# Kernel tuning notes

Measured on AMD Instinct MI355X. Metric: run time of the kernel, lower is better.

The kernel has to match this reference:

```python
import jax, jax.numpy as jnp
import numpy as np

N, D_IN, D_KQ, D_V = 4096, 1024, 1024, 1024


def setup_inputs() -> dict:
    key = jax.random.key(0)
    kx, kq, kk, kv = jax.random.split(key, 4)
    return {
        "x": jax.random.normal(kx, (N, D_IN), dtype=jnp.float32),
        "W_query": jax.random.uniform(kq, (D_IN, D_KQ), dtype=jnp.float32),
        "W_key": jax.random.uniform(kk, (D_IN, D_KQ), dtype=jnp.float32),
        "W_value": jax.random.uniform(kv, (D_IN, D_V), dtype=jnp.float32),
        "masked": 1,
    }


def reference(x, W_query, W_key, W_value, masked):
    # x: [N, d_in]; single-head, unbatched attention
    queries = x @ W_query          # [N, d_kq]
    keys = x @ W_key               # [N, d_kq]
    values = x @ W_value           # [N, d_v]
    scores = queries @ keys.T      # [N, N]
    if masked:  # masked is a static Python int
        n = x.shape[0]
        causal = jnp.triu(jnp.ones((n, n), dtype=bool), k=1)
        scores = jnp.where(causal, -jnp.inf, scores)
    scale = 1.0 / jnp.sqrt(jnp.asarray(W_key.shape[1], dtype=scores.dtype))
    attn = jax.nn.softmax(scores * scale, axis=-1)
    return attn @ values           # [N, d_v]
```

## Files before the change

kernel.cpp:

```cpp
#include <hip/hip_runtime.h>
#include <hip/hip_bf16.h>


using bf16 = __hip_bfloat16;
using f32x4 = __attribute__((ext_vector_type(4))) float;
using i32x4 = __attribute__((ext_vector_type(4))) int;
using i8 = signed char;

__device__ __forceinline__ void gload_lds16(const void* g, void* l) {
  __builtin_amdgcn_global_load_lds(
      (const __attribute__((address_space(1))) void*)g,
      (__attribute__((address_space(3))) void*)l, 16, 0, 0);
}

template <int ROWS, int CPR, int NT>
__device__ __forceinline__ void stage_tile8(const i8* __restrict__ g, i8* s,
                                            int ld) {
  const int t = threadIdx.x;
#pragma unroll
  for (int c = 0; c < ROWS * CPR / NT; ++c) {
    const int idx = c * NT + t;
    const int row = idx / CPR;
    const int ch = idx & (CPR - 1);
    const int cg = ch ^ ((row >> 1) & (CPR - 1));
    gload_lds16(g + (size_t)row * ld + cg * 16, s + idx * 16);
  }
}
template <int CPR>
__device__ __forceinline__ i32x4 frag_at8(const i8* s, int row, int ch) {
  return *(const i32x4*)&s[(row * CPR + (ch ^ ((row >> 1) & (CPR - 1)))) * 16];
}

__device__ __forceinline__ i32x4 mfma_i8(i32x4 a, i32x4 b, i32x4 c) {
  return __builtin_amdgcn_mfma_i32_16x16x64_i8(a, b, c, 0, 0, 0);
}

__device__ __forceinline__ void wait_vm6() {
  asm volatile("s_waitcnt vmcnt(6)" ::: "memory");
}
__device__ __forceinline__ void wait_vm3() {
  asm volatile("s_waitcnt vmcnt(3)" ::: "memory");
}
__device__ __forceinline__ void wait_vm0() {
  asm volatile("s_waitcnt vmcnt(0)" ::: "memory");
}
__device__ __forceinline__ void barrier_pipe() {
  __builtin_amdgcn_s_barrier();
  __builtin_amdgcn_sched_barrier(0);
}

__global__ __launch_bounds__(256, 3) void gemm_qkv_i8(
    const i8* __restrict__ xh, const i8* __restrict__ xl,
    const i8* __restrict__ qTh, const i8* __restrict__ qTl,
    const i8* __restrict__ kTh, const i8* __restrict__ kTl,
    const i8* __restrict__ vTh, const i8* __restrict__ vTl,
    const float* __restrict__ srow, i8* __restrict__ Qh, i8* __restrict__ Ql,
    i8* __restrict__ Kh, i8* __restrict__ Kl, i8* __restrict__ VT) {
  __shared__ __align__(16) i8 sAh[2][128 * 64], sAl[2][128 * 64];
  __shared__ __align__(16) i8 sBh[2][64 * 64], sBl[2][64 * 64];

  const int bx = blockIdx.x;
  const int which = bx >> 4;
  const int n0 = (bx & 15) * 64;
  const int m0 = blockIdx.y * 128;
  const i8* Bh = which == 0 ? qTh : which == 1 ? kTh : vTh;
  const i8* Bl = which == 0 ? qTl : which == 1 ? kTl : vTl;
  const i8* A_h = xh + (size_t)m0 * 1024;
  const i8* A_l = xl + (size_t)m0 * 1024;
  const i8* B_h = Bh + (size_t)n0 * 1024;
  const i8* B_l = Bl + (size_t)n0 * 1024;

  const int t = threadIdx.x, lane = t & 63, w = t >> 6;
  const int wr = (w >> 1) * 64, wc = (w & 1) * 32;
  const int frow = lane & 15, fc = lane >> 4;

  i32x4 a0[4][2], a1[4][2];
#pragma unroll
  for (int i = 0; i < 4; ++i)
#pragma unroll
    for (int j = 0; j < 2; ++j) {
      a0[i][j] = (i32x4){0, 0, 0, 0};
      a1[i][j] = (i32x4){0, 0, 0, 0};
    }

  auto stage_all = [&](int kt, int b) {
    const int k0 = kt * 64;
    stage_tile8<128, 4, 256>(A_h + k0, sAh[b], 1024);
    stage_tile8<64, 4, 256>(B_h + k0, sBh[b], 1024);
    stage_tile8<128, 4, 256>(A_l + k0, sAl[b], 1024);
    stage_tile8<64, 4, 256>(B_l + k0, sBl[b], 1024);
  };

  stage_all(0, 0);
  for (int kt = 0; kt < 16; ++kt) {
    const int cur = kt & 1;
    if (kt < 15) {
      stage_all(kt + 1, cur ^ 1);
      wait_vm6();
    } else {
      wait_vm0();
    }
    barrier_pipe();

    i32x4 ah[4], al[4], bh[2], bl[2];
#pragma unroll
    for (int i = 0; i < 4; ++i) {
      ah[i] = frag_at8<4>(sAh[cur], wr + i * 16 + frow, fc);
      al[i] = frag_at8<4>(sAl[cur], wr + i * 16 + frow, fc);
    }
#pragma unroll
    for (int j = 0; j < 2; ++j) {
      bh[j] = frag_at8<4>(sBh[cur], wc + j * 16 + frow, fc);
      bl[j] = frag_at8<4>(sBl[cur], wc + j * 16 + frow, fc);
    }

    __builtin_amdgcn_s_setprio(1);
#pragma unroll
    for (int i = 0; i < 4; ++i)
#pragma unroll
      for (int j = 0; j < 2; ++j) {
        a0[i][j] = mfma_i8(ah[i], bh[j], a0[i][j]);
        a1[i][j] = mfma_i8(ah[i], bl[j], a1[i][j]);
        a1[i][j] = mfma_i8(al[i], bh[j], a1[i][j]);
      }
    __builtin_amdgcn_s_setprio(0);
    barrier_pipe();
  }

  const int er = (lane >> 4) * 4, ec = lane & 15;
  if (which < 2) {
    i8* Ph = which == 0 ? Qh : Kh;
    i8* Pl = which == 0 ? Ql : Kl;
#pragma unroll
    for (int i = 0; i < 4; ++i)
#pragma unroll
      for (int j = 0; j < 2; ++j)
#pragma unroll
        for (int r = 0; r < 4; ++r) {
          const int gm = m0 + wr + i * 16 + er + r;
          const int gn = n0 + wc + j * 16 + ec;
          const float Qf =
              65536.f * (float)a0[i][j][r] + 256.f * (float)a1[i][j][r];
          int q16 = __float2int_rn(Qf * (1.f / 262144.f));
          q16 = min(max(q16, -32511), 32511);
          const int h = (q16 + 128) >> 8;
          const int l = q16 - (h << 8);
          const size_t off = (size_t)gm * 1024 + gn;
          Ph[off] = (i8)h;
          Pl[off] = (i8)l;
        }
  } else {
    const int gm_base = m0 + wr;
#pragma unroll
    for (int i = 0; i < 4; ++i)
#pragma unroll
      for (int j = 0; j < 2; ++j) {
        const int gn = n0 + wc + j * 16 + ec;
        uint pk = 0;
#pragma unroll
        for (int r = 0; r < 4; ++r) {
          const int gm = gm_base + i * 16 + er + r;
          const float Vf =
              (65536.f * (float)a0[i][j][r] + 256.f * (float)a1[i][j][r]) *
                  (1.f / 134217728.f) +
              0.5f * srow[gm];
          int v8 = __float2int_rn(Vf);
          v8 = min(max(v8, -127), 127);
          pk |= (uint)(v8 & 255) << (8 * r);
        }
        *(uint*)(VT + (size_t)gn * 4096 + gm_base + i * 16 + er) = pk;
      }
  }
}

__global__ __launch_bounds__(256, 3) void gemm_s_i8(
    const i8* __restrict__ Qh, const i8* __restrict__ Ql,
    const i8* __restrict__ Kh, const i8* __restrict__ Kl,
    const float* __restrict__ srow, const float* __restrict__ qsum,
    const float* __restrict__ ksum, float* __restrict__ S) {
  const int u = blockIdx.x;
  int rb = (int)((sqrtf(4.f * (float)u + 1.f) - 1.f) * 0.5f);
  while ((rb + 1) * (rb + 2) <= u) ++rb;
  while (rb * (rb + 1) > u) --rb;
  const int cb = u - rb * (rb + 1);
  const int n0 = cb * 64, m0 = rb * 128;
  __shared__ __align__(16) i8 sAh[2][128 * 64], sAl[2][128 * 64];
  __shared__ __align__(16) i8 sBh[2][64 * 64], sBl[2][64 * 64];

  const i8* A_h = Qh + (size_t)m0 * 1024;
  const i8* A_l = Ql + (size_t)m0 * 1024;
  const i8* B_h = Kh + (size_t)n0 * 1024;
  const i8* B_l = Kl + (size_t)n0 * 1024;

  const int t = threadIdx.x, lane = t & 63, w = t >> 6;
  const int wr = (w >> 1) * 64, wc = (w & 1) * 32;
  const int frow = lane & 15, fc = lane >> 4;

  i32x4 a0[4][2], a1[4][2];
#pragma unroll
  for (int i = 0; i < 4; ++i)
#pragma unroll
    for (int j = 0; j < 2; ++j) {
      a0[i][j] = (i32x4){0, 0, 0, 0};
      a1[i][j] = (i32x4){0, 0, 0, 0};
    }

  auto stage_all = [&](int kt, int b) {
    const int k0 = kt * 64;
    stage_tile8<128, 4, 256>(A_h + k0, sAh[b], 1024);
    stage_tile8<64, 4, 256>(B_h + k0, sBh[b], 1024);
    stage_tile8<128, 4, 256>(A_l + k0, sAl[b], 1024);
    stage_tile8<64, 4, 256>(B_l + k0, sBl[b], 1024);
  };

  stage_all(0, 0);
  for (int kt = 0; kt < 16; ++kt) {
    const int cur = kt & 1;
    if (kt < 15) {
      stage_all(kt + 1, cur ^ 1);
      wait_vm6();
    } else {
      wait_vm0();
    }
    barrier_pipe();

    i32x4 ah[4], al[4], bh[2], bl[2];
#pragma unroll
    for (int i = 0; i < 4; ++i) {
      ah[i] = frag_at8<4>(sAh[cur], wr + i * 16 + frow, fc);
      al[i] = frag_at8<4>(sAl[cur], wr + i * 16 + frow, fc);
    }
#pragma unroll
    for (int j = 0; j < 2; ++j) {
      bh[j] = frag_at8<4>(sBh[cur], wc + j * 16 + frow, fc);
      bl[j] = frag_at8<4>(sBl[cur], wc + j * 16 + frow, fc);
    }

    __builtin_amdgcn_s_setprio(1);
#pragma unroll
    for (int i = 0; i < 4; ++i)
#pragma unroll
      for (int j = 0; j < 2; ++j) {
        a0[i][j] = mfma_i8(ah[i], bh[j], a0[i][j]);
        a1[i][j] = mfma_i8(ah[i], bl[j], a1[i][j]);
        a1[i][j] = mfma_i8(al[i], bh[j], a1[i][j]);
      }
    __builtin_amdgcn_s_setprio(0);
    barrier_pipe();
  }

  const int er = (lane >> 4) * 4, ec = lane & 15;
  float sn[2], kn[2];
#pragma unroll
  for (int j = 0; j < 2; ++j) {
    const int gn = n0 + wc + j * 16 + ec;
    sn[j] = srow[gn];
    kn[j] = ksum[gn];
  }
#pragma unroll
  for (int i = 0; i < 4; ++i)
#pragma unroll
    for (int r = 0; r < 4; ++r) {
      const int gm = m0 + wr + i * 16 + er + r;
      const float sm = srow[gm], qm = qsum[gm];
#pragma unroll
      for (int j = 0; j < 2; ++j) {
        const int gn = n0 + wc + j * 16 + ec;
        const float Sf =
            65536.f * (float)a0[i][j][r] + 256.f * (float)a1[i][j][r];
        const float logit = Sf * (1.f / 8388608.f) +
                            0.015625f * (sn[j] * qm + sm * kn[j]) +
                            8.f * sm * sn[j];
        S[(size_t)gm * 4096 + gn] = logit;
      }
    }
}

__global__ __launch_bounds__(256, 4) void gemm_pv_i8(
    const i8* __restrict__ P, const i8* __restrict__ VT,
    const float* __restrict__ inv_s, float* __restrict__ O) {
  __shared__ __align__(16) i8 sP[2][128 * 64];
  __shared__ __align__(16) i8 sV[2][64 * 64];

  const int cid = blockIdx.x;
  const int h = cid >> 8;
  const int idx = cid & 255;
  const int rb = h ? (31 - (idx >> 3)) : (idx >> 3);
  const int m0 = rb * 128;
  const int n0 = ((idx & 7) + 8 * h) * 64;
  const int ktiles = 2 * (rb + 1);

  const i8* A0 = P + (size_t)m0 * 4096;
  const i8* B0 = VT + (size_t)n0 * 4096;

  const int t = threadIdx.x, lane = t & 63, w = t >> 6;
  const int wr = (w >> 1) * 64, wc = (w & 1) * 32;
  const int frow = lane & 15, fc = lane >> 4;

  i32x4 a0[4][2];
#pragma unroll
  for (int i = 0; i < 4; ++i)
#pragma unroll
    for (int j = 0; j < 2; ++j) a0[i][j] = (i32x4){0, 0, 0, 0};

  auto stage_all = [&](int kt, int b) {
    const int k0 = kt * 64;
    stage_tile8<128, 4, 256>(A0 + k0, sP[b], 4096);
    stage_tile8<64, 4, 256>(B0 + k0, sV[b], 4096);
  };

  stage_all(0, 0);
  for (int kt = 0; kt < ktiles; ++kt) {
    const int cur = kt & 1;
    if (kt + 1 < ktiles) {
      stage_all(kt + 1, cur ^ 1);
      wait_vm3();
    } else {
      wait_vm0();
    }
    barrier_pipe();

    i32x4 pa[4], b[2];
#pragma unroll
    for (int i = 0; i < 4; ++i)
      pa[i] = frag_at8<4>(sP[cur], wr + i * 16 + frow, fc);
#pragma unroll
    for (int j = 0; j < 2; ++j)
      b[j] = frag_at8<4>(sV[cur], wc + j * 16 + frow, fc);

    __builtin_amdgcn_s_setprio(1);
#pragma unroll
    for (int i = 0; i < 4; ++i)
#pragma unroll
      for (int j = 0; j < 2; ++j) a0[i][j] = mfma_i8(pa[i], b[j], a0[i][j]);
    __builtin_amdgcn_s_setprio(0);
    barrier_pipe();
  }

  const int er = (lane >> 4) * 4, ec = lane & 15;
#pragma unroll
  for (int i = 0; i < 4; ++i)
#pragma unroll
    for (int j = 0; j < 2; ++j)
#pragma unroll
      for (int r = 0; r < 4; ++r) {
        const int gm = m0 + wr + i * 16 + er + r;
        const int gn = n0 + wc + j * 16 + ec;
        O[(size_t)gm * 1024 + gn] =
            (float)a0[i][j][r] * inv_s[gm] * (1.f / 127.f);
      }
}

__global__ __launch_bounds__(256) void softmax_kernel(
    const float* __restrict__ S, i8* __restrict__ P,
    float* __restrict__ inv_s, int N) {
  const int wid = threadIdx.x >> 6;
  const int r0 = blockIdx.x * 2 + (wid >> 1);
  const int row = (wid & 1) ? (N - 1 - r0) : r0;
  const int lane = threadIdx.x & 63;
  const float* s = S + (size_t)row * N;
  i8* p = P + (size_t)row * N;
  const int len = row + 1;
  const int nv4 = len >> 2;
  const float4* s4 = (const float4*)s;

  float m = -3.4e38f;
  for (int j = lane; j < nv4; j += 64) {
    const float4 v = s4[j];
    m = fmaxf(m, fmaxf(fmaxf(v.x, v.y), fmaxf(v.z, v.w)));
  }
  for (int j = (nv4 << 2) + lane; j < len; j += 64) m = fmaxf(m, s[j]);
#pragma unroll
  for (int off = 32; off > 0; off >>= 1) m = fmaxf(m, __shfl_xor(m, off, 64));

  float sum = 0.f;
  for (int j = lane; j < nv4; j += 64) {
    const float4 v = s4[j];
    const float e0 = __expf(v.x - m), e1 = __expf(v.y - m);
    const float e2 = __expf(v.z - m), e3 = __expf(v.w - m);
    sum += (e0 + e1) + (e2 + e3);
    uint pk = (uint)__float2int_rn(e0 * 127.f);
    pk |= (uint)__float2int_rn(e1 * 127.f) << 8;
    pk |= (uint)__float2int_rn(e2 * 127.f) << 16;
    pk |= (uint)__float2int_rn(e3 * 127.f) << 24;
    *(uint*)(p + 4 * j) = pk;
  }
  for (int j = (nv4 << 2) + lane; j < len; j += 64) {
    const float e = __expf(s[j] - m);
    sum += e;
    p[j] = (i8)__float2int_rn(e * 127.f);
  }
#pragma unroll
  for (int off = 32; off > 0; off >>= 1) sum += __shfl_xor(sum, off, 64);

  const int bound = ((row >> 7) + 1) << 7;
  for (int j = len + lane; j < bound; j += 64) p[j] = (i8)0;
  if (lane == 0) inv_s[row] = 1.f / sum;
}

__global__ __launch_bounds__(256) void fused_x_rowstats(
    const float* __restrict__ x, const float* __restrict__ wqrow,
    const float* __restrict__ wkrow, uint* __restrict__ xh,
    uint* __restrict__ xl, float* __restrict__ srow, float* __restrict__ qsum,
    float* __restrict__ ksum) {
  const int row = blockIdx.x * 4 + (threadIdx.x >> 6);
  const int lane = threadIdx.x & 63;
  const float4* r4 = (const float4*)(x + (size_t)row * 1024);
  const float4* wq4 = (const float4*)wqrow;
  const float4* wk4 = (const float4*)wkrow;
  uint* h4 = xh + (size_t)row * 256;
  uint* l4 = xl + (size_t)row * 256;

  float ss = 0.f, sq = 0.f, sk = 0.f;
  for (int j = lane; j < 256; j += 64) {
    const float4 v = r4[j];
    const float4 wq = wq4[j];
    const float4 wk = wk4[j];
    const float f[4] = {v.x, v.y, v.z, v.w};
    ss += (v.x + v.y) + (v.z + v.w);
    sq += v.x * wq.x + v.y * wq.y + v.z * wq.z + v.w * wq.w;
    sk += v.x * wk.x + v.y * wk.y + v.z * wk.z + v.w * wk.w;
    uint hp = 0, lp = 0;
#pragma unroll
    for (int k = 0; k < 4; ++k) {
      int q = __float2int_rn(f[k] * 4096.f);
      q = min(max(q, -32511), 32511);
      const int hh = (q + 128) >> 8;
      const int ll = q - (hh << 8);
      hp |= (uint)(hh & 255) << (8 * k);
      lp |= (uint)(ll & 255) << (8 * k);
    }
    h4[j] = hp;
    l4[j] = lp;
  }
#pragma unroll
  for (int off = 32; off > 0; off >>= 1) {
    ss += __shfl_xor(ss, off, 64);
    sq += __shfl_xor(sq, off, 64);
    sk += __shfl_xor(sk, off, 64);
  }
  if (lane == 0) {
    srow[row] = ss;
    qsum[row] = sq;
    ksum[row] = sk;
  }
}

__global__ void split_transpose_w_i8(
    const float* __restrict__ W0, const float* __restrict__ W1,
    const float* __restrict__ W2, i8* __restrict__ T0h, i8* __restrict__ T0l,
    i8* __restrict__ T1h, i8* __restrict__ T1l, i8* __restrict__ T2h,
    i8* __restrict__ T2l, int R, int C) {
  const int z = blockIdx.z;
  const float* W = z == 0 ? W0 : z == 1 ? W1 : W2;
  i8* Th = z == 0 ? T0h : z == 1 ? T1h : T2h;
  i8* Tl = z == 0 ? T0l : z == 1 ? T1l : T2l;
  __shared__ float tile[32][33];
  const int c0 = blockIdx.x * 32, r0 = blockIdx.y * 32;
  const int tx = threadIdx.x, ty = threadIdx.y;
  for (int rr = ty; rr < 32; rr += 8)
    tile[rr][tx] = W[(size_t)(r0 + rr) * C + c0 + tx];
  __syncthreads();
  for (int cc = ty; cc < 32; cc += 8) {
    const float v = tile[tx][cc] - 0.5f;
    int w16 = __float2int_rn(v * 32768.f);
    w16 = min(max(w16, -32511), 32511);
    const int h = (w16 + 128) >> 8;
    const int l = w16 - (h << 8);
    const size_t off = (size_t)(c0 + cc) * R + r0 + tx;
    Th[off] = (i8)h;
    Tl[off] = (i8)l;
  }
}

__global__ __launch_bounds__(256) void wrow_kernel(const float* __restrict__ Wq,
                                                   const float* __restrict__ Wk,
                                                   float* __restrict__ wqrow,
                                                   float* __restrict__ wkrow) {
  const int k = blockIdx.x * 4 + (threadIdx.x >> 6);
  const int lane = threadIdx.x & 63;
  const float* W = blockIdx.y == 0 ? Wq : Wk;
  float* out = blockIdx.y == 0 ? wqrow : wkrow;
  const float* row = W + (size_t)k * 1024;
  float s = 0.f;
  for (int c = lane; c < 1024; c += 64) s += row[c];
#pragma unroll
  for (int off = 32; off > 0; off >>= 1) s += __shfl_xor(s, off, 64);
  if (lane == 0) out[k] = s - 512.f;
}

extern "C" void kernel_launch(void* const* d_in, const int* in_sizes, int n_in,
                              void* d_out, int out_size, void* d_ws,
                              size_t ws_size, hipStream_t stream) {
  (void)in_sizes; (void)n_in; (void)out_size; (void)ws_size;
  const float* x = (const float*)d_in[0];
  const float* Wq = (const float*)d_in[1];
  const float* Wk = (const float*)d_in[2];
  const float* Wv = (const float*)d_in[3];

  const int N = 4096, D = 1024;

  char* p = (char*)d_ws;
  auto alloc = [&](size_t bytes) {
    char* r = p;
    p += (bytes + 255) & ~(size_t)255;
    return r;
  };
  i8* xh = (i8*)alloc((size_t)N * D);
  i8* xl = (i8*)alloc((size_t)N * D);
  i8* WqTh = (i8*)alloc((size_t)D * D);
  i8* WqTl = (i8*)alloc((size_t)D * D);
  i8* WkTh = (i8*)alloc((size_t)D * D);
  i8* WkTl = (i8*)alloc((size_t)D * D);
  i8* WvTh = (i8*)alloc((size_t)D * D);
  i8* WvTl = (i8*)alloc((size_t)D * D);
  i8* Qh = (i8*)alloc((size_t)N * D);
  i8* Ql = (i8*)alloc((size_t)N * D);
  i8* Kh = (i8*)alloc((size_t)N * D);
  i8* Kl = (i8*)alloc((size_t)N * D);
  i8* VT = (i8*)alloc((size_t)D * N);
  float* S = (float*)alloc((size_t)N * N * 4);
  i8* P = (i8*)alloc((size_t)N * N);
  float* inv_s = (float*)alloc((size_t)N * 4);
  float* srow = (float*)alloc((size_t)N * 4);
  float* qsum = (float*)alloc((size_t)N * 4);
  float* ksum = (float*)alloc((size_t)N * 4);
  float* wqrow = (float*)alloc((size_t)D * 4);
  float* wkrow = (float*)alloc((size_t)D * 4);

  wrow_kernel<<<dim3(D / 4, 2), 256, 0, stream>>>(Wq, Wk, wqrow, wkrow);
  split_transpose_w_i8<<<dim3(32, 32, 3), dim3(32, 8), 0, stream>>>(
      Wq, Wk, Wv, WqTh, WqTl, WkTh, WkTl, WvTh, WvTl, D, D);
  fused_x_rowstats<<<N / 4, 256, 0, stream>>>(x, wqrow, wkrow, (uint*)xh,
                                              (uint*)xl, srow, qsum, ksum);

  gemm_qkv_i8<<<dim3(48, 32), 256, 0, stream>>>(xh, xl, WqTh, WqTl, WkTh, WkTl,
                                                WvTh, WvTl, srow, Qh, Ql, Kh,
                                                Kl, VT);

  gemm_s_i8<<<1056, 256, 0, stream>>>(Qh, Ql, Kh, Kl, srow, qsum, ksum, S);

  softmax_kernel<<<N / 4, 256, 0, stream>>>(S, P, inv_s, N);

  gemm_pv_i8<<<512, 256, 0, stream>>>(P, VT, inv_s, (float*)d_out);
}
```

Before: 225.2 us.

## Move V projection into softmax launch to overlap compute-bound GEMM with memory-bound softmax

Splits the QKV projection so the first GEMM computes only Q and K. The V projection now runs as 512 extra blocks inside a combined kernel alongside the 1024 softmax blocks. The goal is to overlap the MFMA-heavy V GEMM with the bandwidth-bound softmax pass over S and fill the GPU better. The cost is that the softmax blocks now inherit the GEMM's large LDS allocation and launch bounds, which can lower their occupancy.

```diff
diff --git a/kernel.cpp b/kernel.cpp
--- a/kernel.cpp
+++ b/kernel.cpp
@@ -49,13 +49,12 @@
   __builtin_amdgcn_sched_barrier(0);
 }
 
-__global__ __launch_bounds__(256, 3) void gemm_qkv_i8(
+__global__ __launch_bounds__(256, 3) void gemm_qk_i8(
     const i8* __restrict__ xh, const i8* __restrict__ xl,
     const i8* __restrict__ qTh, const i8* __restrict__ qTl,
     const i8* __restrict__ kTh, const i8* __restrict__ kTl,
-    const i8* __restrict__ vTh, const i8* __restrict__ vTl,
-    const float* __restrict__ srow, i8* __restrict__ Qh, i8* __restrict__ Ql,
-    i8* __restrict__ Kh, i8* __restrict__ Kl, i8* __restrict__ VT) {
+    i8* __restrict__ Qh, i8* __restrict__ Ql, i8* __restrict__ Kh,
+    i8* __restrict__ Kl) {
   __shared__ __align__(16) i8 sAh[2][128 * 64], sAl[2][128 * 64];
   __shared__ __align__(16) i8 sBh[2][64 * 64], sBl[2][64 * 64];
 
@@ -63,8 +62,8 @@
   const int which = bx >> 4;
   const int n0 = (bx & 15) * 64;
   const int m0 = blockIdx.y * 128;
-  const i8* Bh = which == 0 ? qTh : which == 1 ? kTh : vTh;
-  const i8* Bl = which == 0 ? qTl : which == 1 ? kTl : vTl;
+  const i8* Bh = which == 0 ? qTh : kTh;
+  const i8* Bl = which == 0 ? qTl : kTl;
   const i8* A_h = xh + (size_t)m0 * 1024;
   const i8* A_l = xl + (size_t)m0 * 1024;
   const i8* B_h = Bh + (size_t)n0 * 1024;
@@ -128,49 +127,26 @@
   }
 
   const int er = (lane >> 4) * 4, ec = lane & 15;
-  if (which < 2) {
-    i8* Ph = which == 0 ? Qh : Kh;
-    i8* Pl = which == 0 ? Ql : Kl;
-#pragma unroll
-    for (int i = 0; i < 4; ++i)
-#pragma unroll
-      for (int j = 0; j < 2; ++j)
-#pragma unroll
-        for (int r = 0; r < 4; ++r) {
-          const int gm = m0 + wr + i * 16 + er + r;
-          const int gn = n0 + wc + j * 16 + ec;
-          const float Qf =
-              65536.f * (float)a0[i][j][r] + 256.f * (float)a1[i][j][r];
-          int q16 = __float2int_rn(Qf * (1.f / 262144.f));
-          q16 = min(max(q16, -32511), 32511);
-          const int h = (q16 + 128) >> 8;
-          const int l = q16 - (h << 8);
-          const size_t off = (size_t)gm * 1024 + gn;
-          Ph[off] = (i8)h;
-          Pl[off] = (i8)l;
-        }
-  } else {
-    const int gm_base = m0 + wr;
-#pragma unroll
-    for (int i = 0; i < 4; ++i)
-#pragma unroll
-      for (int j = 0; j < 2; ++j) {
+  i8* Ph = which == 0 ? Qh : Kh;
+  i8* Pl = which == 0 ? Ql : Kl;
+#pragma unroll
+  for (int i = 0; i < 4; ++i)
+#pragma unroll
+    for (int j = 0; j < 2; ++j)
+#pragma unroll
+      for (int r = 0; r < 4; ++r) {
+        const int gm = m0 + wr + i * 16 + er + r;
         const int gn = n0 + wc + j * 16 + ec;
-        uint pk = 0;
-#pragma unroll
-        for (int r = 0; r < 4; ++r) {
-          const int gm = gm_base + i * 16 + er + r;
-          const float Vf =
-              (65536.f * (float)a0[i][j][r] + 256.f * (float)a1[i][j][r]) *
-                  (1.f / 134217728.f) +
-              0.5f * srow[gm];
-          int v8 = __float2int_rn(Vf);
-          v8 = min(max(v8, -127), 127);
-          pk |= (uint)(v8 & 255) << (8 * r);
-        }
-        *(uint*)(VT + (size_t)gn * 4096 + gm_base + i * 16 + er) = pk;
-      }
-  }
+        const float Qf =
+            65536.f * (float)a0[i][j][r] + 256.f * (float)a1[i][j][r];
+        int q16 = __float2int_rn(Qf * (1.f / 262144.f));
+        q16 = min(max(q16, -32511), 32511);
+        const int h = (q16 + 128) >> 8;
+        const int l = q16 - (h << 8);
+        const size_t off = (size_t)gm * 1024 + gn;
+        Ph[off] = (i8)h;
+        Pl[off] = (i8)l;
+      }
 }
 
 __global__ __launch_bounds__(256, 3) void gemm_s_i8(
@@ -276,6 +252,150 @@
     }
 }
 
+__global__ __launch_bounds__(256, 3) void vproj_softmax(
+    const i8* __restrict__ xh, const i8* __restrict__ xl,
+    const i8* __restrict__ vTh, const i8* __restrict__ vTl,
+    const float* __restrict__ srow, i8* __restrict__ VT,
+    const float* __restrict__ S, i8* __restrict__ P,
+    float* __restrict__ inv_s, int N) {
+  __shared__ __align__(16) i8 sAh[2][128 * 64], sAl[2][128 * 64];
+  __shared__ __align__(16) i8 sBh[2][64 * 64], sBl[2][64 * 64];
+
+  if (blockIdx.x < 512) {
+    const int vb = blockIdx.x;
+    const int n0 = (vb & 15) * 64;
+    const int m0 = (vb >> 4) * 128;
+    const i8* A_h = xh + (size_t)m0 * 1024;
+    const i8* A_l = xl + (size_t)m0 * 1024;
+    const i8* B_h = vTh + (size_t)n0 * 1024;
+    const i8* B_l = vTl + (size_t)n0 * 1024;
+
+    const int t = threadIdx.x, lane = t & 63, w = t >> 6;
+    const int wr = (w >> 1) * 64, wc = (w & 1) * 32;
+    const int frow = lane & 15, fc = lane >> 4;
+
+    i32x4 a0[4][2], a1[4][2];
+#pragma unroll
+    for (int i = 0; i < 4; ++i)
+#pragma unroll
+      for (int j = 0; j < 2; ++j) {
+        a0[i][j] = (i32x4){0, 0, 0, 0};
+        a1[i][j] = (i32x4){0, 0, 0, 0};
+      }
+
+    auto stage_all = [&](int kt, int b) {
+      const int k0 = kt * 64;
+      stage_tile8<128, 4, 256>(A_h + k0, sAh[b], 1024);
+      stage_tile8<64, 4, 256>(B_h + k0, sBh[b], 1024);
+      stage_tile8<128, 4, 256>(A_l + k0, sAl[b], 1024);
+      stage_tile8<64, 4, 256>(B_l + k0, sBl[b], 1024);
+    };
+
+    stage_all(0, 0);
+    for (int kt = 0; kt < 16; ++kt) {
+      const int cur = kt & 1;
+      if (kt < 15) {
+        stage_all(kt + 1, cur ^ 1);
+        wait_vm6();
+      } else {
+        wait_vm0();
+      }
+      barrier_pipe();
+
+      i32x4 ah[4], al[4], bh[2], bl[2];
+#pragma unroll
+      for (int i = 0; i < 4; ++i) {
+        ah[i] = frag_at8<4>(sAh[cur], wr + i * 16 + frow, fc);
+        al[i] = frag_at8<4>(sAl[cur], wr + i * 16 + frow, fc);
+      }
+#pragma unroll
+      for (int j = 0; j < 2; ++j) {
+        bh[j] = frag_at8<4>(sBh[cur], wc + j * 16 + frow, fc);
+        bl[j] = frag_at8<4>(sBl[cur], wc + j * 16 + frow, fc);
+      }
+
+      __builtin_amdgcn_s_setprio(1);
+#pragma unroll
+      for (int i = 0; i < 4; ++i)
+#pragma unroll
+        for (int j = 0; j < 2; ++j) {
+          a0[i][j] = mfma_i8(ah[i], bh[j], a0[i][j]);
+          a1[i][j] = mfma_i8(ah[i], bl[j], a1[i][j]);
+          a1[i][j] = mfma_i8(al[i], bh[j], a1[i][j]);
+        }
+      __builtin_amdgcn_s_setprio(0);
+      barrier_pipe();
+    }
+
+    const int er = (lane >> 4) * 4, ec = lane & 15;
+    const int gm_base = m0 + wr;
+#pragma unroll
+    for (int i = 0; i < 4; ++i)
+#pragma unroll
+      for (int j = 0; j < 2; ++j) {
+        const int gn = n0 + wc + j * 16 + ec;
+        uint pk = 0;
+#pragma unroll
+        for (int r = 0; r < 4; ++r) {
+          const int gm = gm_base + i * 16 + er + r;
+          const float Vf =
+              (65536.f * (float)a0[i][j][r] + 256.f * (float)a1[i][j][r]) *
+                  (1.f / 134217728.f) +
+              0.5f * srow[gm];
+          int v8 = __float2int_rn(Vf);
+          v8 = min(max(v8, -127), 127);
+          pk |= (uint)(v8 & 255) << (8 * r);
+        }
+        *(uint*)(VT + (size_t)gn * 4096 + gm_base + i * 16 + er) = pk;
+      }
+  } else {
+    const int sb = blockIdx.x - 512;
+    const int wid = threadIdx.x >> 6;
+    const int r0 = sb * 2 + (wid >> 1);
+    const int row = (wid & 1) ? (N - 1 - r0) : r0;
+    const int lane = threadIdx.x & 63;
+    const float* s = S + (size_t)row * N;
+    i8* p = P + (size_t)row * N;
+    const int len = row + 1;
+    const int nv4 = len >> 2;
+    const float4* s4 = (const float4*)s;
+
+    float m = -3.4e38f;
+    for (int j = lane; j < nv4; j += 64) {
+      const float4 v = s4[j];
+      m = fmaxf(m, fmaxf(fmaxf(v.x, v.y), fmaxf(v.z, v.w)));
+    }
+    for (int j = (nv4 << 2) + lane; j < len; j += 64) m = fmaxf(m, s[j]);
+#pragma unroll
+    for (int off = 32; off > 0; off >>= 1)
+      m = fmaxf(m, __shfl_xor(m, off, 64));
+
+    float sum = 0.f;
+    for (int j = lane; j < nv4; j += 64) {
+      const float4 v = s4[j];
+      const float e0 = __expf(v.x - m), e1 = __expf(v.y - m);
+      const float e2 = __expf(v.z - m), e3 = __expf(v.w - m);
+      sum += (e0 + e1) + (e2 + e3);
+      uint pk = (uint)__float2int_rn(e0 * 127.f);
+      pk |= (uint)__float2int_rn(e1 * 127.f) << 8;
+      pk |= (uint)__float2int_rn(e2 * 127.f) << 16;
+      pk |= (uint)__float2int_rn(e3 * 127.f) << 24;
+      *(uint*)(p + 4 * j) = pk;
+    }
+    for (int j = (nv4 << 2) + lane; j < len; j += 64) {
+      const float e = __expf(s[j] - m);
+      sum += e;
+      p[j] = (i8)__float2int_rn(e * 127.f);
+    }
+#pragma unroll
+    for (int off = 32; off > 0; off >>= 1) sum += __shfl_xor(sum, off, 64);
+
+    const int bound = ((row >> 7) + 1) << 7;
+    for (int j = len + lane; j < bound; j += 64) p[j] = (i8)0;
+    if (lane == 0) inv_s[row] = 1.f / sum;
+  }
+}
+
 __global__ __launch_bounds__(256, 4) void gemm_pv_i8(
     const i8* __restrict__ P, const i8* __restrict__ VT,
     const float* __restrict__ inv_s, float* __restrict__ O) {
@@ -349,53 +469,6 @@
         O[(size_t)gm * 1024 + gn] =
             (float)a0[i][j][r] * inv_s[gm] * (1.f / 127.f);
       }
-}
-
-__global__ __launch_bounds__(256) void softmax_kernel(
-    const float* __restrict__ S, i8* __restrict__ P,
-    float* __restrict__ inv_s, int N) {
-  const int wid = threadIdx.x >> 6;
-  const int r0 = blockIdx.x * 2 + (wid >> 1);
-  const int row = (wid & 1) ? (N - 1 - r0) : r0;
-  const int lane = threadIdx.x & 63;
-  const float* s = S + (size_t)row * N;
-  i8* p = P + (size_t)row * N;
-  const int len = row + 1;
-  const int nv4 = len >> 2;
-  const float4* s4 = (const float4*)s;
-
-  float m = -3.4e38f;
-  for (int j = lane; j < nv4; j += 64) {
-    const float4 v = s4[j];
-    m = fmaxf(m, fmaxf(fmaxf(v.x, v.y), fmaxf(v.z, v.w)));
-  }
-  for (int j = (nv4 << 2) + lane; j < len; j += 64) m = fmaxf(m, s[j]);
-#pragma unroll
-  for (int off = 32; off > 0; off >>= 1) m = fmaxf(m, __shfl_xor(m, off, 64));
-
-  float sum = 0.f;
-  for (int j = lane; j < nv4; j += 64) {
-    const float4 v = s4[j];
-    const float e0 = __expf(v.x - m), e1 = __expf(v.y - m);
-    const float e2 = __expf(v.z - m), e3 = __expf(v.w - m);
-    sum += (e0 + e1) + (e2 + e3);
-    uint pk = (uint)__float2int_rn(e0 * 127.f);
-    pk |= (uint)__float2int_rn(e1 * 127.f) << 8;
-    pk |= (uint)__float2int_rn(e2 * 127.f) << 16;
-    pk |= (uint)__float2int_rn(e3 * 127.f) << 24;
-    *(uint*)(p + 4 * j) = pk;
-  }
-  for (int j = (nv4 << 2) + lane; j < len; j += 64) {
-    const float e = __expf(s[j] - m);
-    sum += e;
-    p[j] = (i8)__float2int_rn(e * 127.f);
-  }
-#pragma unroll
-  for (int off = 32; off > 0; off >>= 1) sum += __shfl_xor(sum, off, 64);
-
-  const int bound = ((row >> 7) + 1) << 7;
-  for (int j = len + lane; j < bound; j += 64) p[j] = (i8)0;
-  if (lane == 0) inv_s[row] = 1.f / sum;
 }
 
 __global__ __launch_bounds__(256) void fused_x_rowstats(
@@ -534,13 +607,13 @@
   fused_x_rowstats<<<N / 4, 256, 0, stream>>>(x, wqrow, wkrow, (uint*)xh,
                                               (uint*)xl, srow, qsum, ksum);
 
-  gemm_qkv_i8<<<dim3(48, 32), 256, 0, stream>>>(xh, xl, WqTh, WqTl, WkTh, WkTl,
-                                                WvTh, WvTl, srow, Qh, Ql, Kh,
-                                                Kl, VT);
+  gemm_qk_i8<<<dim3(32, 32), 256, 0, stream>>>(xh, xl, WqTh, WqTl, WkTh, WkTl,
+                                               Qh, Ql, Kh, Kl);
 
   gemm_s_i8<<<1056, 256, 0, stream>>>(Qh, Ql, Kh, Kl, srow, qsum, ksum, S);
 
-  softmax_kernel<<<N / 4, 256, 0, stream>>>(S, P, inv_s, N);
+  vproj_softmax<<<1536, 256, 0, stream>>>(xh, xl, WvTh, WvTl, srow, VT, S, P,
+                                          inv_s, N);
 
   gemm_pv_i8<<<512, 256, 0, stream>>>(P, VT, inv_s, (float*)d_out);
 }
```

Measured after the change: 230.8 us. +2.5%, slower.
